# Kernel tuning notes

Hardware: AMD Instinct MI355X
Metric: run time of the kernel (lower is better)

Reference implementation:

```python
import jax, jax.numpy as jnp
import numpy as np

B, S, N, C, OUT = 16, 1024, 4096, 768, 256


def setup_inputs() -> dict:
    key = jax.random.key(0)
    k0, k1, k2, k3, k4 = jax.random.split(key, 5)
    seed_xyz = jax.random.normal(k0, (B, S, 3), jnp.float32)   # normalized seed coords
    p_last = jax.random.normal(k1, (B, N, 3), jnp.float32)     # lift3d last-stage coords
    f_last = jax.random.normal(k2, (B, C, N), jnp.float32)     # lift3d last-stage features (channel-first)
    W = jax.random.normal(k3, (OUT, C), jnp.float32) * 0.02    # Conv1d(C, 256, kernel_size=1) weight
    b = jax.random.normal(k4, (OUT,), jnp.float32) * 0.02      # Conv1d bias
    return {"seed_xyz": seed_xyz, "p_last": p_last, "f_last": f_last, "W": W, "b": b}


def reference(seed_xyz, p_last, f_last, W, b):
    # Squared pairwise distances [B,S,N] (argmin invariant to sqrt)
    d2 = (jnp.sum(seed_xyz * seed_xyz, axis=-1, keepdims=True)          # [B,S,1]
          - 2.0 * jnp.einsum('bsd,bnd->bsn', seed_xyz, p_last)          # [B,S,N]
          + jnp.sum(p_last * p_last, axis=-1)[:, None, :])              # [B,1,N]
    idx = jnp.argmin(d2, axis=-1)                                       # [B,S]
    # Gather nearest-neighbor features: [B,C,N] -> [B,C,S]
    gathered = jnp.take_along_axis(f_last, idx[:, None, :], axis=2)
    # 1x1 Conv1d projector: [B,C,S] x [OUT,C] -> [B,OUT,S]
    seed_features = jnp.einsum('bcs,oc->bos', gathered, W) + b[None, :, None]
    return seed_features
```

## Files before the change

kernel.cpp:

```cpp
#include <hip/hip_runtime.h>
#include <stdint.h>

#define B_   16
#define S_   1024
#define N_   4096
#define C_   768
#define OUT_ 256

typedef short bf16x8 __attribute__((ext_vector_type(8)));
typedef float f32x4  __attribute__((ext_vector_type(4)));

#define GLOBAL_AS __attribute__((address_space(1)))
#define LDS_AS    __attribute__((address_space(3)))

__device__ __forceinline__ unsigned short f2bf(float f) {
    unsigned int u = __float_as_uint(f);
    u += 0x7fffu + ((u >> 16) & 1u);
    return (unsigned short)(u >> 16);
}

__device__ __forceinline__ void gl_lds16(const void* gsrc, void* ldst) {
    __builtin_amdgcn_global_load_lds((const GLOBAL_AS void*)gsrc,
                                     (LDS_AS void*)ldst, 16, 0, 0);
}

__global__ __launch_bounds__(256) void k_wconv(const float* __restrict__ W,
                                               unsigned short* __restrict__ Wb) {
    int i = blockIdx.x * 256 + threadIdx.x;
    Wb[i] = f2bf(W[i]);
}

__global__ __launch_bounds__(256) void k_argmin(const float* __restrict__ seed,
                                                const float* __restrict__ pl,
                                                int* __restrict__ idx_out) {
    const int t    = threadIdx.x;
    const int lane = t & 63;
    const int w    = t >> 6;
    const int gw   = blockIdx.x * 4 + w;
    const int b    = gw >> 8;
    const int s0   = (gw & 255) * 4;

    float sx[4], sy[4], sz[4], s2[4], best[4];
    int   bidx[4];
#pragma unroll
    for (int j = 0; j < 4; ++j) {
        const float* sp = seed + (size_t)(b * S_ + s0 + j) * 3;
        sx[j] = sp[0]; sy[j] = sp[1]; sz[j] = sp[2];
        s2[j] = __fadd_rn(__fadd_rn(__fmul_rn(sx[j], sx[j]),
                                    __fmul_rn(sy[j], sy[j])),
                          __fmul_rn(sz[j], sz[j]));
        best[j] = 3.4e38f;
        bidx[j] = 0;
    }
    const float* pb = pl + (size_t)b * N_ * 3;

    for (int k = 0; k < N_ / 64; ++k) {
        const int   n  = k * 64 + lane;
        const float px = pb[n * 3 + 0];
        const float py = pb[n * 3 + 1];
        const float pz = pb[n * 3 + 2];
        const float p2 = __fadd_rn(__fadd_rn(__fmul_rn(px, px),
                                             __fmul_rn(py, py)),
                                   __fmul_rn(pz, pz));
#pragma unroll
        for (int j = 0; j < 4; ++j) {
            float dot = __fadd_rn(__fadd_rn(__fmul_rn(sx[j], px),
                                            __fmul_rn(sy[j], py)),
                                  __fmul_rn(sz[j], pz));
            float d2  = __fadd_rn(__fsub_rn(s2[j], __fmul_rn(2.0f, dot)), p2);
            if (d2 < best[j]) { best[j] = d2; bidx[j] = n; }
        }
    }

#pragma unroll
    for (int j = 0; j < 4; ++j) {
#pragma unroll
        for (int off = 32; off >= 1; off >>= 1) {
            float ob = __shfl_xor(best[j], off, 64);
            int   oi = __shfl_xor(bidx[j], off, 64);
            bool take = (ob < best[j]) || (ob == best[j] && oi < bidx[j]);
            if (take) { best[j] = ob; bidx[j] = oi; }
        }
        if (lane == 0) idx_out[b * S_ + s0 + j] = bidx[j];
    }
}

#define CT 24
__global__ __launch_bounds__(256) void k_gather(const float* __restrict__ f,
                                                const int* __restrict__ idx,
                                                unsigned short* __restrict__ gt) {
    __shared__ unsigned short tile[S_ * (CT + 2)];
    const int t  = threadIdx.x;
    const int b  = blockIdx.x >> 5;
    const int ct = blockIdx.x & 31;
    const int c0 = ct * CT;

    int idxv[4];
#pragma unroll
    for (int j = 0; j < 4; ++j) idxv[j] = idx[b * S_ + t + 256 * j];

    const float* fb = f + ((size_t)b * C_ + c0) * N_;
    for (int i = 0; i < CT; ++i) {
        const float* row = fb + (size_t)i * N_;
        float v0 = row[idxv[0]];
        float v1 = row[idxv[1]];
        float v2 = row[idxv[2]];
        float v3 = row[idxv[3]];
        tile[(t      ) * (CT + 2) + i] = f2bf(v0);
        tile[(t + 256) * (CT + 2) + i] = f2bf(v1);
        tile[(t + 512) * (CT + 2) + i] = f2bf(v2);
        tile[(t + 768) * (CT + 2) + i] = f2bf(v3);
    }
    __syncthreads();

    const size_t ob = (size_t)b * S_ * C_ + c0;
    for (int it = 0; it < 48; ++it) {
        int li = t + it * 256;
        int s  = li / 12;
        int cu = li - s * 12;
        unsigned int v = *(const unsigned int*)&tile[s * (CT + 2) + cu * 2];
        *(unsigned int*)(gt + ob + (size_t)s * C_ + cu * 2) = v;
    }
}

__global__ __launch_bounds__(256) void k_gemm(const unsigned short* __restrict__ Wb,
                                              const unsigned short* __restrict__ gt,
                                              const float* __restrict__ bias,
                                              float* __restrict__ out) {
    __shared__ unsigned short ldsA[128 * 32];
    __shared__ unsigned short ldsB[128 * 32];
    const int t    = threadIdx.x;
    const int bid  = blockIdx.x;
    const int b    = bid >> 4;
    const int mt   = (bid >> 3) & 1;
    const int nt   = bid & 7;
    const int m0   = mt * 128;
    const int n0   = nt * 128;
    const int lane = t & 63;
    const int w    = t >> 6;
    const int wm   = w & 1, wn = w >> 1;
    const int quad = lane >> 4, l16 = lane & 15;

    f32x4 acc[4][4];
#pragma unroll
    for (int i = 0; i < 4; ++i)
#pragma unroll
        for (int j = 0; j < 4; ++j) acc[i][j] = (f32x4){0.f, 0.f, 0.f, 0.f};

    const int rowS = t >> 2;
    const int kkS  = (t & 3) * 8;
    const unsigned short* aSrc0 = Wb + (size_t)(m0 + rowS) * C_ + kkS;
    const unsigned short* aSrc1 = Wb + (size_t)(m0 + 64 + rowS) * C_ + kkS;
    const unsigned short* bBase = gt + (size_t)b * S_ * C_;
    const unsigned short* bSrc0 = bBase + (size_t)(n0 + rowS) * C_ + kkS;
    const unsigned short* bSrc1 = bBase + (size_t)(n0 + 64 + rowS) * C_ + kkS;
    unsigned short* la = ldsA + t * 8;
    unsigned short* lb = ldsB + t * 8;

    for (int kt = 0; kt < C_ / 32; ++kt) {
        const int k0 = kt * 32;
        gl_lds16(aSrc0 + k0, la);
        gl_lds16(aSrc1 + k0, la + 2048);
        gl_lds16(bSrc0 + k0, lb);
        gl_lds16(bSrc1 + k0, lb + 2048);
        __syncthreads();

        bf16x8 aF[4], bF[4];
#pragma unroll
        for (int mi = 0; mi < 4; ++mi)
            aF[mi] = *(const bf16x8*)(ldsA + ((wm * 64 + mi * 16 + l16) * 32 + quad * 8));
#pragma unroll
        for (int ni = 0; ni < 4; ++ni)
            bF[ni] = *(const bf16x8*)(ldsB + ((wn * 64 + ni * 16 + l16) * 32 + quad * 8));
#pragma unroll
        for (int mi = 0; mi < 4; ++mi)
#pragma unroll
            for (int ni = 0; ni < 4; ++ni)
                acc[mi][ni] = __builtin_amdgcn_mfma_f32_16x16x32_bf16(
                    aF[mi], bF[ni], acc[mi][ni], 0, 0, 0);
        __syncthreads();
    }

    float* obase = out + (size_t)b * OUT_ * S_;
#pragma unroll
    for (int mi = 0; mi < 4; ++mi) {
#pragma unroll
        for (int r = 0; r < 4; ++r) {
            const int o  = m0 + wm * 64 + mi * 16 + quad * 4 + r;
            const float bo = bias[o];
            float* orow = obase + (size_t)o * S_;
#pragma unroll
            for (int ni = 0; ni < 4; ++ni) {
                const int s = n0 + wn * 64 + ni * 16 + l16;
                orow[s] = acc[mi][ni][r] + bo;
            }
        }
    }
}

extern "C" void kernel_launch(void* const* d_in, const int* in_sizes, int n_in,
                              void* d_out, int out_size, void* d_ws, size_t ws_size,
                              hipStream_t stream) {
    const float* seed = (const float*)d_in[0];
    const float* pl   = (const float*)d_in[1];
    const float* f    = (const float*)d_in[2];
    const float* W    = (const float*)d_in[3];
    const float* bias = (const float*)d_in[4];
    float* out = (float*)d_out;

    int* idx            = (int*)d_ws;
    unsigned short* Wb  = (unsigned short*)((char*)d_ws + 65536);
    unsigned short* gt  = (unsigned short*)((char*)d_ws + 524288);

    k_wconv <<<768,  256, 0, stream>>>(W, Wb);
    k_argmin<<<1024, 256, 0, stream>>>(seed, pl, idx);
    k_gather<<<512,  256, 0, stream>>>(f, idx, gt);
    k_gemm  <<<256,  256, 0, stream>>>(Wb, gt, bias, out);
}
```

Baseline: 366.5 us.

## Stream full feature rows into LDS with double buffering for gather

The gather kernel now copies each full 4096-float feature row into LDS with coalesced async global-to-LDS loads, double-buffered across 8 channels per block, and then gathers from LDS instead of doing random global reads. Each thread packs its 8 bf16 channels into registers and writes them as one 16-byte store, which removes the transposition tile. The grid triples to 1536 blocks with 32KB of LDS each. The cost is reading every feature row in full rather than only the indexed entries, though random 4-byte global reads waste most of each cache line anyway.

Result: faster. 359.1 us (-2.0%).

```diff
diff --git a/kernel.cpp b/kernel.cpp
--- a/kernel.cpp
+++ b/kernel.cpp
@@ -85,14 +85,14 @@
     }
 }
 
-#define CT 24
+#define CT 8
 __global__ __launch_bounds__(256) void k_gather(const float* __restrict__ f,
                                                 const int* __restrict__ idx,
                                                 unsigned short* __restrict__ gt) {
-    __shared__ unsigned short tile[S_ * (CT + 2)];
+    __shared__ float buf[2][N_];
     const int t  = threadIdx.x;
-    const int b  = blockIdx.x >> 5;
-    const int ct = blockIdx.x & 31;
+    const int b  = blockIdx.x / 96;
+    const int ct = blockIdx.x % 96;
     const int c0 = ct * CT;
 
     int idxv[4];
@@ -100,26 +100,34 @@
     for (int j = 0; j < 4; ++j) idxv[j] = idx[b * S_ + t + 256 * j];
 
     const float* fb = f + ((size_t)b * C_ + c0) * N_;
-    for (int i = 0; i < CT; ++i) {
-        const float* row = fb + (size_t)i * N_;
-        float v0 = row[idxv[0]];
-        float v1 = row[idxv[1]];
-        float v2 = row[idxv[2]];
-        float v3 = row[idxv[3]];
-        tile[(t      ) * (CT + 2) + i] = f2bf(v0);
-        tile[(t + 256) * (CT + 2) + i] = f2bf(v1);
-        tile[(t + 512) * (CT + 2) + i] = f2bf(v2);
-        tile[(t + 768) * (CT + 2) + i] = f2bf(v3);
-    }
-    __syncthreads();
+
+#pragma unroll
+    for (int k = 0; k < 4; ++k)
+        gl_lds16(fb + t * 4 + k * 1024, &buf[0][t * 4 + k * 1024]);
+
+    unsigned short og[4][CT] __attribute__((aligned(16)));
+
+#pragma unroll
+    for (int j = 0; j < CT; ++j) {
+        __syncthreads();
+        if (j + 1 < CT) {
+            const float* row = fb + (size_t)(j + 1) * N_;
+            float* dst = &buf[(j + 1) & 1][0];
+#pragma unroll
+            for (int k = 0; k < 4; ++k)
+                gl_lds16(row + t * 4 + k * 1024, dst + t * 4 + k * 1024);
+        }
+        const float* src = &buf[j & 1][0];
+#pragma unroll
+        for (int si = 0; si < 4; ++si)
+            og[si][j] = f2bf(src[idxv[si]]);
+    }
 
     const size_t ob = (size_t)b * S_ * C_ + c0;
-    for (int it = 0; it < 48; ++it) {
-        int li = t + it * 256;
-        int s  = li / 12;
-        int cu = li - s * 12;
-        unsigned int v = *(const unsigned int*)&tile[s * (CT + 2) + cu * 2];
-        *(unsigned int*)(gt + ob + (size_t)s * C_ + cu * 2) = v;
+#pragma unroll
+    for (int si = 0; si < 4; ++si) {
+        int s = t + si * 256;
+        *(uint4*)(gt + ob + (size_t)s * C_) = *(const uint4*)og[si];
     }
 }
 
@@ -214,6 +222,6 @@
 
     k_wconv <<<768,  256, 0, stream>>>(W, Wb);
     k_argmin<<<1024, 256, 0, stream>>>(seed, pl, idx);
-    k_gather<<<512,  256, 0, stream>>>(f, idx, gt);
+    k_gather<<<1536, 256, 0, stream>>>(f, idx, gt);
     k_gemm  <<<256,  256, 0, stream>>>(Wb, gt, bias, out);
 }
```

## Replace random-column gather with full coalesced transpose and row-gather inside GEMM

Applied to the files above, without the earlier changes.

Transposes all of f_last into a [B,N,C] bf16 buffer with coalesced tiled loads, then has the GEMM load B-operand rows directly via the nearest-neighbor indices. This removes the strided, uncoalesced per-channel column gather. In exchange it reads and writes the entire feature tensor rather than only selected columns, and needs a much larger workspace.

Result: faster. 356.4 us (-2.8%).

```diff
diff --git a/kernel.cpp b/kernel.cpp
--- a/kernel.cpp
+++ b/kernel.cpp
@@ -85,46 +85,38 @@
     }
 }
 
-#define CT 24
-__global__ __launch_bounds__(256) void k_gather(const float* __restrict__ f,
-                                                const int* __restrict__ idx,
-                                                unsigned short* __restrict__ gt) {
-    __shared__ unsigned short tile[S_ * (CT + 2)];
+__global__ __launch_bounds__(256) void k_transpose(const float* __restrict__ f,
+                                                   unsigned short* __restrict__ ft) {
+    __shared__ unsigned short tl[64][72];
     const int t  = threadIdx.x;
-    const int b  = blockIdx.x >> 5;
-    const int ct = blockIdx.x & 31;
-    const int c0 = ct * CT;
-
-    int idxv[4];
-#pragma unroll
-    for (int j = 0; j < 4; ++j) idxv[j] = idx[b * S_ + t + 256 * j];
-
-    const float* fb = f + ((size_t)b * C_ + c0) * N_;
-    for (int i = 0; i < CT; ++i) {
-        const float* row = fb + (size_t)i * N_;
-        float v0 = row[idxv[0]];
-        float v1 = row[idxv[1]];
-        float v2 = row[idxv[2]];
-        float v3 = row[idxv[3]];
-        tile[(t      ) * (CT + 2) + i] = f2bf(v0);
-        tile[(t + 256) * (CT + 2) + i] = f2bf(v1);
-        tile[(t + 512) * (CT + 2) + i] = f2bf(v2);
-        tile[(t + 768) * (CT + 2) + i] = f2bf(v3);
+    const int nt = blockIdx.x & 63;
+    const int ct = (blockIdx.x >> 6) % 12;
+    const int b  = blockIdx.x / 768;
+    const int c0 = ct * 64, n0 = nt * 64;
+
+    const float* fb = f + ((size_t)b * C_ + c0) * N_ + n0;
+#pragma unroll
+    for (int r = 0; r < 4; ++r) {
+        const int c  = (t >> 4) + 16 * r;
+        const int nn = (t & 15) * 4;
+        f32x4 v = *(const f32x4*)(fb + (size_t)c * N_ + nn);
+#pragma unroll
+        for (int i = 0; i < 4; ++i) tl[nn + i][c] = f2bf(v[i]);
     }
     __syncthreads();
 
-    const size_t ob = (size_t)b * S_ * C_ + c0;
-    for (int it = 0; it < 48; ++it) {
-        int li = t + it * 256;
-        int s  = li / 12;
-        int cu = li - s * 12;
-        unsigned int v = *(const unsigned int*)&tile[s * (CT + 2) + cu * 2];
-        *(unsigned int*)(gt + ob + (size_t)s * C_ + cu * 2) = v;
-    }
+    const int n  = t >> 2;
+    const int c8 = (t & 3) * 16;
+    uint4 o0 = *(const uint4*)&tl[n][c8];
+    uint4 o1 = *(const uint4*)&tl[n][c8 + 8];
+    unsigned short* od = ft + ((size_t)(b * N_ + n0 + n)) * C_ + c0 + c8;
+    *(uint4*)(od)     = o0;
+    *(uint4*)(od + 8) = o1;
 }
 
 __global__ __launch_bounds__(256) void k_gemm(const unsigned short* __restrict__ Wb,
-                                              const unsigned short* __restrict__ gt,
+                                              const unsigned short* __restrict__ ft,
+                                              const int* __restrict__ idx,
                                               const float* __restrict__ bias,
                                               float* __restrict__ out) {
     __shared__ unsigned short ldsA[128 * 32];
@@ -151,18 +143,23 @@
     const int kkS  = (t & 3) * 8;
     const unsigned short* aSrc0 = Wb + (size_t)(m0 + rowS) * C_ + kkS;
     const unsigned short* aSrc1 = Wb + (size_t)(m0 + 64 + rowS) * C_ + kkS;
-    const unsigned short* bBase = gt + (size_t)b * S_ * C_;
-    const unsigned short* bSrc0 = bBase + (size_t)(n0 + rowS) * C_ + kkS;
-    const unsigned short* bSrc1 = bBase + (size_t)(n0 + 64 + rowS) * C_ + kkS;
+
+    const unsigned short* ftB = ft + (size_t)b * N_ * C_;
+    const int nB0 = idx[b * S_ + n0 + rowS];
+    const int nB1 = idx[b * S_ + n0 + 64 + rowS];
+    const unsigned short* bSrc0 = ftB + (size_t)nB0 * C_ + kkS;
+    const unsigned short* bSrc1 = ftB + (size_t)nB1 * C_ + kkS;
+
     unsigned short* la = ldsA + t * 8;
-    unsigned short* lb = ldsB + t * 8;
 
     for (int kt = 0; kt < C_ / 32; ++kt) {
         const int k0 = kt * 32;
         gl_lds16(aSrc0 + k0, la);
         gl_lds16(aSrc1 + k0, la + 2048);
-        gl_lds16(bSrc0 + k0, lb);
-        gl_lds16(bSrc1 + k0, lb + 2048);
+        bf16x8 bv0 = *(const bf16x8*)(bSrc0 + k0);
+        bf16x8 bv1 = *(const bf16x8*)(bSrc1 + k0);
+        *(bf16x8*)(ldsB + t * 8)        = bv0;
+        *(bf16x8*)(ldsB + 2048 + t * 8) = bv1;
         __syncthreads();
 
         bf16x8 aF[4], bF[4];
@@ -210,10 +207,10 @@
 
     int* idx            = (int*)d_ws;
     unsigned short* Wb  = (unsigned short*)((char*)d_ws + 65536);
-    unsigned short* gt  = (unsigned short*)((char*)d_ws + 524288);
-
-    k_wconv <<<768,  256, 0, stream>>>(W, Wb);
-    k_argmin<<<1024, 256, 0, stream>>>(seed, pl, idx);
-    k_gather<<<512,  256, 0, stream>>>(f, idx, gt);
-    k_gemm  <<<256,  256, 0, stream>>>(Wb, gt, bias, out);
-}
+    unsigned short* ft  = (unsigned short*)((char*)d_ws + 524288);
+
+    k_wconv    <<<768,   256, 0, stream>>>(W, Wb);
+    k_argmin   <<<1024,  256, 0, stream>>>(seed, pl, idx);
+    k_transpose<<<12288, 256, 0, stream>>>(f, ft);
+    k_gemm     <<<256,   256, 0, stream>>>(Wb, ft, idx, bias, out);
+}
```
